# Kernel tuning notes

Hardware: AMD Instinct MI355X
Metric: run time of the kernel (lower is better)

The kernel has to match this reference:

```python
import jax, jax.numpy as jnp
import numpy as np

N, E, F, D, H, HID, OUT, G = 25000, 400000, 128, 16, 64, 128, 32, 64

def silu(v):
    return v * jax.nn.sigmoid(v)

def setup_inputs() -> dict:
    key = jax.random.key(0)
    ks = jax.random.split(key, 32)
    inp = {
        'x': jax.random.normal(ks[0], (N, F), jnp.float32),
        'pos': jax.random.normal(ks[1], (N, 3), jnp.float32),
        'edge_attr': jax.random.normal(ks[2], (E, D), jnp.float32),
        'edge_index': jax.random.randint(ks[3], (2, E), 0, N, jnp.int64),
        'batch': jnp.sort(jax.random.randint(ks[4], (N,), 0, G, jnp.int64)),
    }
    def lin(k, fan_in, fan_out):
        return jax.random.normal(k, (fan_in, fan_out), jnp.float32) / np.sqrt(fan_in)
    i = 5
    for l, in_c in enumerate([F, HID]):
        cat = 2 * in_c + D + 1
        inp[f'l{l}_mlp_w'] = lin(ks[i], cat, H); i += 1
        inp[f'l{l}_edge_w'] = lin(ks[i], H, H); i += 1
        inp[f'l{l}_edge_b'] = jnp.zeros((H,), jnp.float32)
        inp[f'l{l}_coord_w'] = lin(ks[i], H, 1); i += 1
        inp[f'l{l}_coord_b'] = jnp.zeros((1,), jnp.float32)
        inp[f'l{l}_node_w1'] = lin(ks[i], in_c + H, H); i += 1
        inp[f'l{l}_node_b1'] = jnp.zeros((H,), jnp.float32)
        inp[f'l{l}_node_w2'] = lin(ks[i], H, HID); i += 1
        inp[f'l{l}_node_b2'] = jnp.zeros((HID,), jnp.float32)
    inp['out_w1'] = lin(ks[i], HID, HID); i += 1
    inp['out_b1'] = jnp.zeros((HID,), jnp.float32)
    inp['out_w2'] = lin(ks[i], HID, OUT); i += 1
    inp['out_b2'] = jnp.zeros((OUT,), jnp.float32)
    return inp

def egnn_layer(x, pos, src, dst, edge_attr, mlp_w, edge_w, edge_b, coord_w, coord_b, nw1, nb1, nw2, nb2):
    # PyG flow source_to_target: i = dst (edge_index[1]), j = src (edge_index[0])
    diff = pos[dst] - pos[src]                    # (E,3)
    radial = jnp.sum(diff * diff, axis=1, keepdims=True)  # (E,1)
    cat = jnp.concatenate([x[dst], x[src], edge_attr, radial], axis=1)
    h = silu(cat @ mlp_w)                         # (E,H)
    e_ij = silu(h @ edge_w + edge_b)              # (E,H)
    coord_update = diff * silu(e_ij @ coord_w + coord_b)  # (E,3)
    e_agg = jax.ops.segment_sum(e_ij, dst, num_segments=N)          # sum reduce
    cu_sum = jax.ops.segment_sum(coord_update, dst, num_segments=N)
    deg = jax.ops.segment_sum(jnp.ones((E, 1), x.dtype), dst, num_segments=N)
    cu_mean = cu_sum / jnp.maximum(deg, 1.0)      # mean reduce, 0 for isolated nodes
    h_node = silu(jnp.concatenate([x, e_agg], axis=1) @ nw1 + nb1) @ nw2 + nb2
    return h_node, pos + cu_mean

def reference(x, pos, edge_attr, edge_index, batch,
              l0_mlp_w, l0_edge_w, l0_edge_b, l0_coord_w, l0_coord_b, l0_node_w1, l0_node_b1, l0_node_w2, l0_node_b2,
              l1_mlp_w, l1_edge_w, l1_edge_b, l1_coord_w, l1_coord_b, l1_node_w1, l1_node_b1, l1_node_w2, l1_node_b2,
              out_w1, out_b1, out_w2, out_b2):
    src, dst = edge_index[0], edge_index[1]
    x, pos = egnn_layer(x, pos, src, dst, edge_attr, l0_mlp_w, l0_edge_w, l0_edge_b, l0_coord_w, l0_coord_b, l0_node_w1, l0_node_b1, l0_node_w2, l0_node_b2)
    x, pos = egnn_layer(x, pos, src, dst, edge_attr, l1_mlp_w, l1_edge_w, l1_edge_b, l1_coord_w, l1_coord_b, l1_node_w1, l1_node_b1, l1_node_w2, l1_node_b2)
    # graph mean pooling over batch assignment
    g_sum = jax.ops.segment_sum(x, batch, num_segments=G)
    g_cnt = jax.ops.segment_sum(jnp.ones((N, 1), x.dtype), batch, num_segments=G)
    g = g_sum / jnp.maximum(g_cnt, 1.0)           # (G, HID)
    g = jax.nn.relu(g)
    return jax.nn.relu(g @ out_w1 + out_b1) @ out_w2 + out_b2  # (G, OUT)
```

## Files before the change

kernel.cpp:

```cpp
#include <hip/hip_runtime.h>
#include <math.h>

#define NN 25000
#define EE 400000
#define FF 128
#define DD 16
#define HH 64
#define HIDC 128
#define OUTC 32
#define GG 64
#define NODEBLK 782
#define SCATBLK 1563
#define NTILES 1563

#define EDGEBLK 1792
#define EW_Q 3
#define EW_R 3496

#define WQ_NW1 0
#define WQ_NW2 24576
#define WQ_WN  40960
#define WQ_EW  73728
#define WQ_W3  77824
#define WQ_LAYER 81920

typedef __attribute__((ext_vector_type(8))) short short8;
typedef __attribute__((ext_vector_type(8))) unsigned short u16x8;
typedef __attribute__((ext_vector_type(4))) float f32x4;

union S8 { short8 v; unsigned short u[8]; };
union U8 { u16x8 v; unsigned short u[8]; };

__device__ __forceinline__ float silu_f(float v) {
    return v / (1.f + __expf(-v));
}

__device__ __forceinline__ unsigned short f2bf_rne(float f) {
  unsigned u = __float_as_uint(f);
  unsigned r = u + 0x7fffu + ((u >> 16) & 1u);
  return (unsigned short)(r >> 16);
}
__device__ __forceinline__ float bfbits2f(unsigned short b) {
  return __uint_as_float(((unsigned)b) << 16);
}

__device__ __forceinline__ void split8(const float* hv, S8& hi, S8& lo) {
#pragma unroll
  for (int j = 0; j < 8; ++j) {
    const unsigned short hb = (unsigned short)(__float_as_uint(hv[j]) >> 16);
    hi.u[j] = hb;
    lo.u[j] = f2bf_rne(hv[j] - bfbits2f(hb));
  }
}

__device__ __forceinline__ f32x4 mfma3(const S8& ah, const S8& al,
                                       const S8& bh, const S8& bl, f32x4 c) {
  c = __builtin_amdgcn_mfma_f32_16x16x32_bf16(ah.v, bh.v, c, 0, 0, 0);
  c = __builtin_amdgcn_mfma_f32_16x16x32_bf16(al.v, bh.v, c, 0, 0, 0);
  c = __builtin_amdgcn_mfma_f32_16x16x32_bf16(ah.v, bl.v, c, 0, 0, 0);
  return c;
}

__device__ __forceinline__ void prepSplit(unsigned short* dst, const float* __restrict__ W,
                                          int ldw, int k0, int n0, int q, int m, int lane) {
  S8 hi, lo;
#pragma unroll
  for (int j = 0; j < 8; ++j) {
    const float wv = W[(size_t)(k0 + q * 8 + j) * ldw + n0 + m];
    const unsigned short hb = (unsigned short)(__float_as_uint(wv) >> 16);
    hi.u[j] = hb;
    lo.u[j] = f2bf_rne(wv - bfbits2f(hb));
  }
  *(short8*)(dst + lane * 8) = hi.v;
  *(short8*)(dst + 512 + lane * 8) = lo.v;
}

__device__ __forceinline__ void prepB16(unsigned short* dst, const float* __restrict__ W,
                                        int ldw, int k0, int n0, int q, int m, int lane,
                                        bool zero) {
  S8 b;
#pragma unroll
  for (int j = 0; j < 8; ++j)
    b.u[j] = zero ? (unsigned short)0
                  : f2bf_rne(W[(size_t)(k0 + q * 8 + j) * ldw + n0 + m]);
  *(short8*)(dst + lane * 8) = b.v;
}

__global__ __launch_bounds__(256) void k_hist(
    const int* __restrict__ ei, int* __restrict__ cnt,
    const float* __restrict__ nw1_0, const float* __restrict__ nw2_0,
    const float* __restrict__ mlp0, const float* __restrict__ ew0,
    const float* __restrict__ nw1_1, const float* __restrict__ nw2_1,
    const float* __restrict__ mlp1, const float* __restrict__ ew1,
    unsigned short* __restrict__ wq) {
  if (blockIdx.x < SCATBLK) {
    const int t = blockIdx.x * 256 + threadIdx.x;
    if (t < EE) atomicAdd(&cnt[ei[EE + t]], 1);
    return;
  }
  const int l = blockIdx.x - SCATBLK;
  const float* nw1 = l ? nw1_1 : nw1_0;
  const float* nw2 = l ? nw2_1 : nw2_0;
  const float* mlw = l ? mlp1 : mlp0;
  const float* ew  = l ? ew1 : ew0;
  unsigned short* base = wq + (size_t)l * WQ_LAYER;
  const int tid = threadIdx.x, w = tid >> 6, lane = tid & 63;
  const int q = lane >> 4, m = lane & 15;
  for (int f = w; f < 24; f += 4)
    prepSplit(base + WQ_NW1 + f * 1024, nw1, 64, (f % 6) * 32, (f / 6) * 16, q, m, lane);
  for (int f = w; f < 16; f += 4)
    prepSplit(base + WQ_NW2 + f * 1024, nw2, 128, (f & 1) * 32, (f >> 1) * 16, q, m, lane);
  if (l == 0) {
    for (int f = w; f < 32; f += 4) {
      const int nc = f >> 2, kc = f & 3;
      prepSplit(base + WQ_WN + f * 1024, mlp1 + (size_t)(nc < 4 ? 0 : 128 * 64), 64,
                kc * 32, (nc & 3) * 16, q, m, lane);
    }
  }
  for (int f = w; f < 8; f += 4)
    prepB16(base + WQ_EW + f * 512, ew, 64, (f >> 2) * 32, (f & 3) * 16, q, m, lane, false);
  for (int f = w; f < 4; f += 4)
    prepB16(base + WQ_W3 + f * 512, mlw + 256 * 64, 64, 0, f * 16, q, m, lane, lane >= 32);
}

__global__ __launch_bounds__(1024) void k_scan(
    const int* __restrict__ cnt, int* __restrict__ row_ptr, int* __restrict__ next) {
  __shared__ int s[1024];
  const int t = threadIdx.x;
  const int base = t * 25;
  int loc[25];
  int sum = 0;
#pragma unroll
  for (int i = 0; i < 25; ++i) {
    const int n = base + i;
    loc[i] = (n < NN) ? cnt[n] : 0;
    sum += loc[i];
  }
  s[t] = sum;
  __syncthreads();
  for (int off = 1; off < 1024; off <<= 1) {
    const int v = (t >= off) ? s[t - off] : 0;
    __syncthreads();
    s[t] += v;
    __syncthreads();
  }
  int run = s[t] - sum;
#pragma unroll
  for (int i = 0; i < 25; ++i) {
    const int n = base + i;
    if (n < NN) {
      row_ptr[n] = run;
      next[n] = run;
      run += loc[i];
    }
  }
  if (t == 0) row_ptr[NN] = EE;
}

__global__ __launch_bounds__(256) void k_sp(
    const int* __restrict__ ei, int* __restrict__ next,
    int* __restrict__ sdst, int* __restrict__ ssrc, int* __restrict__ seid,
    const float* __restrict__ X, const float* __restrict__ W,
    float* __restrict__ P1, unsigned short* __restrict__ P2h) {
  __shared__ __align__(16) float xT[4][128 * 12];
  if (blockIdx.x >= NODEBLK) {
    const int t = (blockIdx.x - NODEBLK) * 256 + threadIdx.x;
    if (t < EE) {
      const int d = ei[EE + t];
      const int slot = atomicAdd(&next[d], 1);
      sdst[slot] = d;
      ssrc[slot] = ei[t];
      seid[slot] = t;
    }
    return;
  }
  const int w = threadIdx.x >> 6, lane = threadIdx.x & 63;
  float* xt = xT[w];
  const int nb = (blockIdx.x * 4 + w) * 8;
#pragma unroll
  for (int e = 0; e < 8; ++e) {
    const int n = nb + e;
    const bool v = n < NN;
    xt[lane * 12 + e]        = v ? X[n * FF + lane] : 0.f;
    xt[(lane + 64) * 12 + e] = v ? X[n * FF + 64 + lane] : 0.f;
  }
  __syncthreads();
  float a1[8], a2[8];
#pragma unroll
  for (int e = 0; e < 8; ++e) { a1[e] = 0.f; a2[e] = 0.f; }
#pragma unroll 4
  for (int k = 0; k < 128; ++k) {
    const float wa = W[k * 64 + lane];
    const float wb = W[(128 + k) * 64 + lane];
    float xk[8];
    *(f32x4*)&xk[0] = *(const f32x4*)&xt[k * 12];
    *(f32x4*)&xk[4] = *(const f32x4*)&xt[k * 12 + 4];
#pragma unroll
    for (int e = 0; e < 8; ++e) {
      a1[e] = fmaf(xk[e], wa, a1[e]);
      a2[e] = fmaf(xk[e], wb, a2[e]);
    }
  }
#pragma unroll
  for (int e = 0; e < 8; ++e) {
    const int n = nb + e;
    if (n < NN) {
      P1[n * 64 + lane]  = a1[e];
      P2h[n * 64 + lane] = f2bf_rne(a2[e]);
    }
  }
}

template <bool COORD, bool GATHER>
__global__ __launch_bounds__(256, 4) void k_edge(
    const float* __restrict__ P1, const unsigned short* __restrict__ P2h,
    const float* __restrict__ pos, const float* __restrict__ eattr,
    unsigned short* __restrict__ seattr_h, const int* __restrict__ seid,
    const int* __restrict__ sdst, const int* __restrict__ ssrc,
    const unsigned short* __restrict__ wq, const float* __restrict__ mlp_w,
    const float* __restrict__ edge_b,
    const float* __restrict__ coord_w, const float* __restrict__ coord_b,
    float* __restrict__ e_agg, float* __restrict__ cu) {
  __shared__ __align__(16) float s_hs[4][16 * 76];
  __shared__ float s_diff[4][48];
  __shared__ float s_rad[4][16];
  __shared__ float s_red[4][16];
  const int tid = threadIdx.x, w = tid >> 6, lane = tid & 63;
  const int q = lane >> 4, m = lane & 15;

  S8 wB[2][4];
#pragma unroll
  for (int kc = 0; kc < 2; ++kc)
#pragma unroll
    for (int nc = 0; nc < 4; ++nc)
      wB[kc][nc].v = *(const short8*)(wq + WQ_EW + (kc * 4 + nc) * 512 + lane * 8);
  S8 w3B[4];
#pragma unroll
  for (int nc = 0; nc < 4; ++nc)
    w3B[nc].v = *(const short8*)(wq + WQ_W3 + nc * 512 + lane * 8);
  float w4r[4], cwr[4], ebr[4];
#pragma unroll
  for (int nc = 0; nc < 4; ++nc) {
    w4r[nc] = mlp_w[272 * 64 + nc * 16 + m];
    ebr[nc] = edge_b[nc * 16 + m];
    cwr[nc] = COORD ? coord_w[nc * 16 + m] : 0.f;
  }
  const float cb = COORD ? coord_b[0] : 0.f;

  const int wave_id = blockIdx.x * 4 + w;
  const int g0 = wave_id * EW_Q + (wave_id < EW_R ? wave_id : EW_R);
  const int ng = EW_Q + (wave_id < EW_R ? 1 : 0);

  const int pe = (lane < 48) ? (lane / 3) : 0;
  const int pc = lane - (lane / 3) * 3;

  int cur_dst = -1;
  float accum = 0.f;

  for (int g = 0; g < ng; ++g) {
    const int eb = (g0 + g) * 16;
    const int dm = sdst[eb + m];
    const int sm = ssrc[eb + m];
    f32x4 p1a[2], p1b[2];
    U8 p2r[2];
#pragma unroll
    for (int kc = 0; kc < 2; ++kc) {
      const float* pp1 = P1 + (size_t)dm * 64 + kc * 32 + q * 8;
      p1a[kc] = *(const f32x4*)pp1;
      p1b[kc] = *(const f32x4*)(pp1 + 4);
      p2r[kc].v = *(const u16x8*)(P2h + (size_t)sm * 64 + kc * 32 + q * 8);
    }
    if (lane < 48) {
      const int de = __shfl(dm, pe, 64), se = __shfl(sm, pe, 64);
      s_diff[w][lane] = pos[de * 3 + pc] - pos[se * 3 + pc];
    }
    S8 eaA;
#pragma unroll
    for (int j = 0; j < 8; ++j) eaA.u[j] = 0;
    if (lane < 32) {
      if (GATHER) {
        const int eid = seid[eb + m];
        const float* ep = &eattr[(size_t)eid * DD + q * 8];
        const f32x4 ea0 = *(const f32x4*)ep;
        const f32x4 ea1 = *(const f32x4*)(ep + 4);
#pragma unroll
        for (int j = 0; j < 4; ++j) {
          eaA.u[j]     = f2bf_rne(ea0[j]);
          eaA.u[4 + j] = f2bf_rne(ea1[j]);
        }
        *(short8*)&seattr_h[(size_t)(eb + m) * DD + q * 8] = eaA.v;
      } else {
        eaA.v = *(const short8*)&seattr_h[(size_t)(eb + m) * DD + q * 8];
      }
    }
    if (lane < 16) {
      const float d0 = s_diff[w][lane * 3 + 0];
      const float d1 = s_diff[w][lane * 3 + 1];
      const float d2 = s_diff[w][lane * 3 + 2];
      s_rad[w][lane] = fmaf(d0, d0, fmaf(d1, d1, d2 * d2));
    }
    float radr[4];
#pragma unroll
    for (int r = 0; r < 4; ++r) radr[r] = s_rad[w][q * 4 + r];
    f32x4 c3[4];
#pragma unroll
    for (int nc = 0; nc < 4; ++nc) {
      f32x4 z = {0.f, 0.f, 0.f, 0.f};
      c3[nc] = __builtin_amdgcn_mfma_f32_16x16x32_bf16(eaA.v, w3B[nc].v, z, 0, 0, 0);
    }
#pragma unroll
    for (int nc = 0; nc < 4; ++nc)
#pragma unroll
      for (int r = 0; r < 4; ++r)
        s_hs[w][(q * 4 + r) * 76 + nc * 16 + m] = fmaf(radr[r], w4r[nc], c3[nc][r]);
    S8 ahi[2], alo[2];
#pragma unroll
    for (int kc = 0; kc < 2; ++kc) {
      const float* hp = &s_hs[w][m * 76 + kc * 32 + q * 8];
      f32x4 h0 = *(const f32x4*)hp;
      f32x4 h1 = *(const f32x4*)(hp + 4);
      h0 = h0 + p1a[kc];
      h1 = h1 + p1b[kc];
      float hv[8];
      *(f32x4*)&hv[0] = h0;
      *(f32x4*)&hv[4] = h1;
#pragma unroll
      for (int j = 0; j < 8; ++j) {
        const float h = silu_f(hv[j] + bfbits2f(p2r[kc].u[j]));
        const unsigned short hb = (unsigned short)(__float_as_uint(h) >> 16);
        ahi[kc].u[j] = hb;
        alo[kc].u[j] = f2bf_rne(h - bfbits2f(hb));
      }
    }
    f32x4 o[4];
#pragma unroll
    for (int nc = 0; nc < 4; ++nc) {
      f32x4 bi = {ebr[nc], ebr[nc], ebr[nc], ebr[nc]};
      o[nc] = bi;
    }
#pragma unroll
    for (int kc = 0; kc < 2; ++kc)
#pragma unroll
      for (int nc = 0; nc < 4; ++nc) {
        o[nc] = __builtin_amdgcn_mfma_f32_16x16x32_bf16(ahi[kc].v, wB[kc][nc].v, o[nc], 0, 0, 0);
        o[nc] = __builtin_amdgcn_mfma_f32_16x16x32_bf16(alo[kc].v, wB[kc][nc].v, o[nc], 0, 0, 0);
      }
#pragma unroll
    for (int nc = 0; nc < 4; ++nc)
#pragma unroll
      for (int r = 0; r < 4; ++r) o[nc][r] = silu_f(o[nc][r]);
    if (COORD) {
#pragma unroll
      for (int r = 0; r < 4; ++r) {
        float v = o[0][r] * cwr[0] + o[1][r] * cwr[1] + o[2][r] * cwr[2] + o[3][r] * cwr[3];
        v += __shfl_xor(v, 1, 64);
        v += __shfl_xor(v, 2, 64);
        v += __shfl_xor(v, 4, 64);
        v += __shfl_xor(v, 8, 64);
        if (m == 0) s_red[w][q * 4 + r] = v;
      }
    }
#pragma unroll
    for (int nc = 0; nc < 4; ++nc)
#pragma unroll
      for (int r = 0; r < 4; ++r)
        s_hs[w][(q * 4 + r) * 76 + nc * 16 + m] = o[nc][r];
    for (int e = 0; e < 16; ++e) {
      const int dv = __shfl(dm, e, 64);
      const float v = s_hs[w][e * 76 + lane];
      if (dv == cur_dst) {
        accum += v;
      } else {
        if (cur_dst >= 0) atomicAdd(&e_agg[(size_t)cur_dst * 64 + lane], accum);
        cur_dst = dv;
        accum = v;
      }
    }
    if (COORD) {
      if (lane < 48) {
        const float s = silu_f(s_red[w][pe] + cb);
        atomicAdd(&cu[(size_t)__shfl(dm, pe, 64) * 3 + pc], s_diff[w][lane] * s);
      }
    }
  }
  if (cur_dst >= 0) atomicAdd(&e_agg[(size_t)cur_dst * 64 + lane], accum);
}

template <bool L0>
__global__ __launch_bounds__(256) void k_node(
    const float* __restrict__ x_in, float* __restrict__ e_agg,
    const unsigned short* __restrict__ wq,
    const float* __restrict__ nb1, const float* __restrict__ nb2,
    const float* __restrict__ pos_in, const float* __restrict__ cu,
    const int* __restrict__ row_ptr,
    float* __restrict__ x_out, float* __restrict__ pos_out,
    float* __restrict__ P1, unsigned short* __restrict__ P2h,
    const int* __restrict__ batch,
    float* __restrict__ g_sum, float* __restrict__ g_cnt) {
  __shared__ __align__(16) float sbuf[4][16 * 132];
  const int tid = threadIdx.x, w = tid >> 6, lane = tid & 63;
  const int q = lane >> 4, m = lane & 15;
  const int tile = blockIdx.x * 4 + w;
  if (tile >= NTILES) return;
  const int n0 = tile * 16;
  const int nm = n0 + m;
  const bool vm = nm < NN;
  float* sb = sbuf[w];

  S8 axh[6], axl[6];
#pragma unroll
  for (int kc = 0; kc < 6; ++kc) {
    float hv[8] = {0.f, 0.f, 0.f, 0.f, 0.f, 0.f, 0.f, 0.f};
    if (vm) {
      const float* src = (kc < 4) ? (x_in + (size_t)nm * HIDC + kc * 32 + q * 8)
                                  : (e_agg + (size_t)nm * 64 + (kc - 4) * 32 + q * 8);
      *(f32x4*)&hv[0] = *(const f32x4*)src;
      *(f32x4*)&hv[4] = *(const f32x4*)(src + 4);
    }
    split8(hv, axh[kc], axl[kc]);
  }
  if (L0 && vm) {
    const f32x4 z = {0.f, 0.f, 0.f, 0.f};
    float* ez = e_agg + (size_t)nm * 64 + q * 8;
    *(f32x4*)ez = z; *(f32x4*)(ez + 4) = z;
    *(f32x4*)(ez + 32) = z; *(f32x4*)(ez + 36) = z;
  }
#pragma unroll
  for (int nc = 0; nc < 4; ++nc) {
    const float b = nb1[nc * 16 + m];
    f32x4 acc = {b, b, b, b};
#pragma unroll
    for (int kc = 0; kc < 6; ++kc) {
      S8 bh, bl;
      const unsigned short* fb = wq + WQ_NW1 + (nc * 6 + kc) * 1024 + lane * 8;
      bh.v = *(const short8*)fb;
      bl.v = *(const short8*)(fb + 512);
      acc = mfma3(axh[kc], axl[kc], bh, bl, acc);
    }
#pragma unroll
    for (int r = 0; r < 4; ++r)
      sb[(q * 4 + r) * 132 + nc * 16 + m] = silu_f(acc[r]);
  }
  S8 ah[2], al[2];
#pragma unroll
  for (int kc = 0; kc < 2; ++kc) {
    float hv[8];
    const float* hp = &sb[m * 132 + kc * 32 + q * 8];
    *(f32x4*)&hv[0] = *(const f32x4*)hp;
    *(f32x4*)&hv[4] = *(const f32x4*)(hp + 4);
    split8(hv, ah[kc], al[kc]);
  }
  f32x4 hh[8];
#pragma unroll
  for (int nc = 0; nc < 8; ++nc) {
    const float b = nb2[nc * 16 + m];
    f32x4 acc = {b, b, b, b};
#pragma unroll
    for (int kc = 0; kc < 2; ++kc) {
      S8 bh, bl;
      const unsigned short* fb = wq + WQ_NW2 + (nc * 2 + kc) * 1024 + lane * 8;
      bh.v = *(const short8*)fb;
      bl.v = *(const short8*)(fb + 512);
      acc = mfma3(ah[kc], al[kc], bh, bl, acc);
    }
    hh[nc] = acc;
  }
  if (L0) {
#pragma unroll
    for (int nc = 0; nc < 8; ++nc)
#pragma unroll
      for (int r = 0; r < 4; ++r) {
        const int n = n0 + q * 4 + r;
        sb[(q * 4 + r) * 132 + nc * 16 + m] = hh[nc][r];
        if (n < NN) x_out[(size_t)n * HIDC + nc * 16 + m] = hh[nc][r];
      }
    if (lane < 48) {
      const int pe2 = lane / 3, pc2 = lane - pe2 * 3;
      const int n = n0 + pe2;
      if (n < NN) {
        const float dg = fmaxf((float)(row_ptr[n + 1] - row_ptr[n]), 1.f);
        pos_out[n * 3 + pc2] = pos_in[n * 3 + pc2] + cu[n * 3 + pc2] / dg;
      }
    }
    S8 a1h[4], a1l[4];
#pragma unroll
    for (int kc = 0; kc < 4; ++kc) {
      float hv[8];
      const float* hp = &sb[m * 132 + kc * 32 + q * 8];
      *(f32x4*)&hv[0] = *(const f32x4*)hp;
      *(f32x4*)&hv[4] = *(const f32x4*)(hp + 4);
      split8(hv, a1h[kc], a1l[kc]);
    }
#pragma unroll
    for (int nc = 0; nc < 8; ++nc) {
      const int ncc = nc & 3;
      f32x4 acc = {0.f, 0.f, 0.f, 0.f};
#pragma unroll
      for (int kc = 0; kc < 4; ++kc) {
        S8 bh, bl;
        const unsigned short* fb = wq + WQ_WN + (nc * 4 + kc) * 1024 + lane * 8;
        bh.v = *(const short8*)fb;
        bl.v = *(const short8*)(fb + 512);
        acc = mfma3(a1h[kc], a1l[kc], bh, bl, acc);
      }
#pragma unroll
      for (int r = 0; r < 4; ++r) {
        const int n = n0 + q * 4 + r;
        if (n < NN) {
          if (nc < 4) P1[(size_t)n * 64 + ncc * 16 + m] = acc[r];
          else        P2h[(size_t)n * 64 + ncc * 16 + m] = f2bf_rne(acc[r]);
        }
      }
    }
  } else {
    int curb = -1;
    float cnt2 = 0.f;
    float pacc[8];
#pragma unroll
    for (int r = 0; r < 4; ++r) {
      const int n = n0 + q * 4 + r;
      if (n < NN) {
        const int bg = batch[n];
        if (bg != curb) {
          if (curb >= 0) {
#pragma unroll
            for (int nc = 0; nc < 8; ++nc)
              atomicAdd(&g_sum[curb * HIDC + nc * 16 + m], pacc[nc]);
            if (m == 0) atomicAdd(&g_cnt[curb], cnt2);
          }
          curb = bg;
#pragma unroll
          for (int nc = 0; nc < 8; ++nc) pacc[nc] = hh[nc][r];
          cnt2 = 1.f;
        } else {
#pragma unroll
          for (int nc = 0; nc < 8; ++nc) pacc[nc] += hh[nc][r];
          cnt2 += 1.f;
        }
      }
    }
    if (curb >= 0) {
#pragma unroll
      for (int nc = 0; nc < 8; ++nc)
        atomicAdd(&g_sum[curb * HIDC + nc * 16 + m], pacc[nc]);
      if (m == 0) atomicAdd(&g_cnt[curb], cnt2);
    }
  }
}

__global__ __launch_bounds__(128) void k_final(
    const float* __restrict__ g_sum, const float* __restrict__ g_cnt,
    const float* __restrict__ w1, const float* __restrict__ b1,
    const float* __restrict__ w2, const float* __restrict__ b2,
    float* __restrict__ out) {
  __shared__ float sg[128];
  __shared__ float sh[128];
  const int g = blockIdx.x, j = threadIdx.x;
  const float c = fmaxf(g_cnt[g], 1.f);
  sg[j] = fmaxf(g_sum[g * HIDC + j] / c, 0.f);
  __syncthreads();
  float a = b1[j];
  for (int k = 0; k < 128; ++k) a += sg[k] * w1[k * 128 + j];
  sh[j] = fmaxf(a, 0.f);
  __syncthreads();
  if (j < OUTC) {
    float o = b2[j];
    for (int k = 0; k < 128; ++k) o += sh[k] * w2[k * OUTC + j];
    out[g * OUTC + j] = o;
  }
}

extern "C" void kernel_launch(void* const* d_in, const int* in_sizes, int n_in,
                              void* d_out, int out_size, void* d_ws, size_t ws_size,
                              hipStream_t stream) {
  const float* x     = (const float*)d_in[0];
  const float* pos   = (const float*)d_in[1];
  const float* eattr = (const float*)d_in[2];
  const int*   ei    = (const int*)d_in[3];
  const int*   batch = (const int*)d_in[4];
  const float* mlp_w[2]   = {(const float*)d_in[5],  (const float*)d_in[14]};
  const float* edge_w[2]  = {(const float*)d_in[6],  (const float*)d_in[15]};
  const float* edge_b[2]  = {(const float*)d_in[7],  (const float*)d_in[16]};
  const float* coord_w[2] = {(const float*)d_in[8],  (const float*)d_in[17]};
  const float* coord_b[2] = {(const float*)d_in[9],  (const float*)d_in[18]};
  const float* nw1[2]     = {(const float*)d_in[10], (const float*)d_in[19]};
  const float* nb1[2]     = {(const float*)d_in[11], (const float*)d_in[20]};
  const float* nw2[2]     = {(const float*)d_in[12], (const float*)d_in[21]};
  const float* nb2[2]     = {(const float*)d_in[13], (const float*)d_in[22]};
  const float* ow1 = (const float*)d_in[23];
  const float* ob1 = (const float*)d_in[24];
  const float* ow2 = (const float*)d_in[25];
  const float* ob2 = (const float*)d_in[26];
  float* out = (float*)d_out;

  char* p = (char*)d_ws;
  auto alloc = [&](size_t bytes) {
    void* r = (void*)p;
    p += (bytes + 255) & ~(size_t)255;
    return r;
  };
  float* P1            = (float*)alloc((size_t)NN * 64 * 4);
  unsigned short* P2h  = (unsigned short*)alloc((size_t)NN * 64 * 2);
  char* zero_base      = p;
  float* e_agg         = (float*)alloc((size_t)NN * 64 * 4);
  float* cu            = (float*)alloc((size_t)NN * 3 * 4);
  float* g_sum         = (float*)alloc((size_t)GG * HIDC * 4);
  float* g_cnt         = (float*)alloc((size_t)GG * 4);
  int* cnt             = (int*)alloc((size_t)NN * 4);
  const size_t zero_sz = (size_t)(p - zero_base);
  int* row_ptr         = (int*)alloc((size_t)(NN + 1) * 4);
  int* nxt             = (int*)alloc((size_t)NN * 4);
  int* sdst            = (int*)alloc((size_t)EE * 4);
  int* ssrc            = (int*)alloc((size_t)EE * 4);
  int* seid            = (int*)alloc((size_t)EE * 4);
  unsigned short* seah = (unsigned short*)alloc((size_t)EE * DD * 2);
  float* x1            = (float*)alloc((size_t)NN * HIDC * 4);
  float* pos1          = (float*)alloc((size_t)NN * 3 * 4);
  unsigned short* wqb  = (unsigned short*)alloc((size_t)2 * WQ_LAYER * 2);

  const int nodeTileBlk = (NTILES + 3) / 4;

  (void)hipMemsetAsync(zero_base, 0, zero_sz, stream);

  k_hist<<<SCATBLK + 2, 256, 0, stream>>>(ei, cnt,
      nw1[0], nw2[0], mlp_w[0], edge_w[0],
      nw1[1], nw2[1], mlp_w[1], edge_w[1], wqb);
  k_scan<<<1, 1024, 0, stream>>>(cnt, row_ptr, nxt);
  k_sp<<<NODEBLK + SCATBLK, 256, 0, stream>>>(ei, nxt, sdst, ssrc, seid,
      x, mlp_w[0], P1, P2h);

  k_edge<true, true><<<EDGEBLK, 256, 0, stream>>>(P1, P2h, pos, eattr,
      seah, seid, sdst, ssrc, wqb, mlp_w[0], edge_b[0],
      coord_w[0], coord_b[0], e_agg, cu);
  k_node<true><<<nodeTileBlk, 256, 0, stream>>>(x, e_agg, wqb, nb1[0], nb2[0],
      pos, cu, row_ptr, x1, pos1, P1, P2h, batch, g_sum, g_cnt);

  k_edge<false, false><<<EDGEBLK, 256, 0, stream>>>(P1, P2h, pos1, eattr,
      seah, seid, sdst, ssrc, wqb + WQ_LAYER, mlp_w[1], edge_b[1],
      coord_w[1], coord_b[1], e_agg, cu);
  k_node<false><<<nodeTileBlk, 256, 0, stream>>>(x1, e_agg, wqb + WQ_LAYER,
      nb1[1], nb2[1], pos1, cu, row_ptr, x1, pos1, P1, P2h,
      batch, g_sum, g_cnt);

  k_final<<<GG, 128, 0, stream>>>(g_sum, g_cnt, ow1, ob1, ow2, ob2, out);
}
```

Baseline: 456.4 us.

## Split node MLP columns across waves, retune edge kernel grid and LDS stride

The node kernel now gives each 16-node tile to a whole block: each of the four waves computes one 16-column slice of the first layer and two slices of the second, sharing the hidden activations through LDS with barriers. This launches four times as many node blocks with less per-wave serial MFMA work. The edge kernel gets more blocks (2048), launch bounds targeting 8 blocks per SM, a blockIdx swizzle across 8 groups (likely XCD-aware), and a tighter LDS row stride of 68. The costs are extra barriers, more redundant A-operand loads per block, and possible register spills from the tighter launch bounds.

After: 664.3 us. 1.46x slower.

```diff
diff --git a/kernel.cpp b/kernel.cpp
--- a/kernel.cpp
+++ b/kernel.cpp
@@ -13,9 +13,10 @@
 #define SCATBLK 1563
 #define NTILES 1563
 
-#define EDGEBLK 1792
+#define EDGEBLK 2048
 #define EW_Q 3
-#define EW_R 3496
+#define EW_R 424
+#define HS_STRIDE 68
 
 #define WQ_NW1 0
 #define WQ_NW2 24576
@@ -212,7 +213,7 @@
 }
 
 template <bool COORD, bool GATHER>
-__global__ __launch_bounds__(256, 4) void k_edge(
+__global__ __launch_bounds__(256, 8) void k_edge(
     const float* __restrict__ P1, const unsigned short* __restrict__ P2h,
     const float* __restrict__ pos, const float* __restrict__ eattr,
     unsigned short* __restrict__ seattr_h, const int* __restrict__ seid,
@@ -221,7 +222,7 @@
     const float* __restrict__ edge_b,
     const float* __restrict__ coord_w, const float* __restrict__ coord_b,
     float* __restrict__ e_agg, float* __restrict__ cu) {
-  __shared__ __align__(16) float s_hs[4][16 * 76];
+  __shared__ __align__(16) float s_hs[4][16 * HS_STRIDE];
   __shared__ float s_diff[4][48];
   __shared__ float s_rad[4][16];
   __shared__ float s_red[4][16];
@@ -247,7 +248,8 @@
   }
   const float cb = COORD ? coord_b[0] : 0.f;
 
-  const int wave_id = blockIdx.x * 4 + w;
+  const int sbid = (blockIdx.x & 7) * (EDGEBLK / 8) + (blockIdx.x >> 3);
+  const int wave_id = sbid * 4 + w;
   const int g0 = wave_id * EW_Q + (wave_id < EW_R ? wave_id : EW_R);
   const int ng = EW_Q + (wave_id < EW_R ? 1 : 0);
 
@@ -312,11 +314,11 @@
     for (int nc = 0; nc < 4; ++nc)
 #pragma unroll
       for (int r = 0; r < 4; ++r)
-        s_hs[w][(q * 4 + r) * 76 + nc * 16 + m] = fmaf(radr[r], w4r[nc], c3[nc][r]);
+        s_hs[w][(q * 4 + r) * HS_STRIDE + nc * 16 + m] = fmaf(radr[r], w4r[nc], c3[nc][r]);
     S8 ahi[2], alo[2];
 #pragma unroll
     for (int kc = 0; kc < 2; ++kc) {
-      const float* hp = &s_hs[w][m * 76 + kc * 32 + q * 8];
+      const float* hp = &s_hs[w][m * HS_STRIDE + kc * 32 + q * 8];
       f32x4 h0 = *(const f32x4*)hp;
       f32x4 h1 = *(const f32x4*)(hp + 4);
       h0 = h0 + p1a[kc];
@@ -364,10 +366,10 @@
     for (int nc = 0; nc < 4; ++nc)
 #pragma unroll
       for (int r = 0; r < 4; ++r)
-        s_hs[w][(q * 4 + r) * 76 + nc * 16 + m] = o[nc][r];
+        s_hs[w][(q * 4 + r) * HS_STRIDE + nc * 16 + m] = o[nc][r];
     for (int e = 0; e < 16; ++e) {
       const int dv = __shfl(dm, e, 64);
-      const float v = s_hs[w][e * 76 + lane];
+      const float v = s_hs[w][e * HS_STRIDE + lane];
       if (dv == cur_dst) {
         accum += v;
       } else {
@@ -397,15 +399,12 @@
     float* __restrict__ P1, unsigned short* __restrict__ P2h,
     const int* __restrict__ batch,
     float* __restrict__ g_sum, float* __restrict__ g_cnt) {
-  __shared__ __align__(16) float sbuf[4][16 * 132];
+  __shared__ __align__(16) float sb[16 * 132];
   const int tid = threadIdx.x, w = tid >> 6, lane = tid & 63;
   const int q = lane >> 4, m = lane & 15;
-  const int tile = blockIdx.x * 4 + w;
-  if (tile >= NTILES) return;
-  const int n0 = tile * 16;
+  const int n0 = blockIdx.x * 16;
   const int nm = n0 + m;
   const bool vm = nm < NN;
-  float* sb = sbuf[w];
 
   S8 axh[6], axl[6];
 #pragma unroll
@@ -419,27 +418,27 @@
     }
     split8(hv, axh[kc], axl[kc]);
   }
-  if (L0 && vm) {
+  {
+    const float b = nb1[w * 16 + m];
+    f32x4 acc = {b, b, b, b};
+#pragma unroll
+    for (int kc = 0; kc < 6; ++kc) {
+      S8 bh, bl;
+      const unsigned short* fb = wq + WQ_NW1 + (w * 6 + kc) * 1024 + lane * 8;
+      bh.v = *(const short8*)fb;
+      bl.v = *(const short8*)(fb + 512);
+      acc = mfma3(axh[kc], axl[kc], bh, bl, acc);
+    }
+#pragma unroll
+    for (int r = 0; r < 4; ++r)
+      sb[(q * 4 + r) * 132 + w * 16 + m] = silu_f(acc[r]);
+  }
+  __syncthreads();
+  if (L0 && vm && w == 3) {
     const f32x4 z = {0.f, 0.f, 0.f, 0.f};
     float* ez = e_agg + (size_t)nm * 64 + q * 8;
     *(f32x4*)ez = z; *(f32x4*)(ez + 4) = z;
     *(f32x4*)(ez + 32) = z; *(f32x4*)(ez + 36) = z;
-  }
-#pragma unroll
-  for (int nc = 0; nc < 4; ++nc) {
-    const float b = nb1[nc * 16 + m];
-    f32x4 acc = {b, b, b, b};
-#pragma unroll
-    for (int kc = 0; kc < 6; ++kc) {
-      S8 bh, bl;
-      const unsigned short* fb = wq + WQ_NW1 + (nc * 6 + kc) * 1024 + lane * 8;
-      bh.v = *(const short8*)fb;
-      bl.v = *(const short8*)(fb + 512);
-      acc = mfma3(axh[kc], axl[kc], bh, bl, acc);
-    }
-#pragma unroll
-    for (int r = 0; r < 4; ++r)
-      sb[(q * 4 + r) * 132 + nc * 16 + m] = silu_f(acc[r]);
   }
   S8 ah[2], al[2];
 #pragma unroll
@@ -450,9 +449,10 @@
     *(f32x4*)&hv[4] = *(const f32x4*)(hp + 4);
     split8(hv, ah[kc], al[kc]);
   }
-  f32x4 hh[8];
-#pragma unroll
-  for (int nc = 0; nc < 8; ++nc) {
+  f32x4 hh[2];
+#pragma unroll
+  for (int i = 0; i < 2; ++i) {
+    const int nc = w + i * 4;
     const float b = nb2[nc * 16 + m];
     f32x4 acc = {b, b, b, b};
 #pragma unroll
@@ -463,18 +463,21 @@
       bl.v = *(const short8*)(fb + 512);
       acc = mfma3(ah[kc], al[kc], bh, bl, acc);
     }
-    hh[nc] = acc;
+    hh[i] = acc;
   }
   if (L0) {
-#pragma unroll
-    for (int nc = 0; nc < 8; ++nc)
+    __syncthreads();
+#pragma unroll
+    for (int i = 0; i < 2; ++i) {
+      const int nc = w + i * 4;
 #pragma unroll
       for (int r = 0; r < 4; ++r) {
         const int n = n0 + q * 4 + r;
-        sb[(q * 4 + r) * 132 + nc * 16 + m] = hh[nc][r];
-        if (n < NN) x_out[(size_t)n * HIDC + nc * 16 + m] = hh[nc][r];
-      }
-    if (lane < 48) {
+        sb[(q * 4 + r) * 132 + nc * 16 + m] = hh[i][r];
+        if (n < NN) x_out[(size_t)n * HIDC + nc * 16 + m] = hh[i][r];
+      }
+    }
+    if (w == 0 && lane < 48) {
       const int pe2 = lane / 3, pc2 = lane - pe2 * 3;
       const int n = n0 + pe2;
       if (n < NN) {
@@ -482,6 +485,7 @@
         pos_out[n * 3 + pc2] = pos_in[n * 3 + pc2] + cu[n * 3 + pc2] / dg;
       }
     }
+    __syncthreads();
     S8 a1h[4], a1l[4];
 #pragma unroll
     for (int kc = 0; kc < 4; ++kc) {
@@ -492,8 +496,8 @@
       split8(hv, a1h[kc], a1l[kc]);
     }
 #pragma unroll
-    for (int nc = 0; nc < 8; ++nc) {
-      const int ncc = nc & 3;
+    for (int i = 0; i < 2; ++i) {
+      const int nc = w + i * 4;
       f32x4 acc = {0.f, 0.f, 0.f, 0.f};
 #pragma unroll
       for (int kc = 0; kc < 4; ++kc) {
@@ -507,15 +511,15 @@
       for (int r = 0; r < 4; ++r) {
         const int n = n0 + q * 4 + r;
         if (n < NN) {
-          if (nc < 4) P1[(size_t)n * 64 + ncc * 16 + m] = acc[r];
-          else        P2h[(size_t)n * 64 + ncc * 16 + m] = f2bf_rne(acc[r]);
+          if (i == 0) P1[(size_t)n * 64 + w * 16 + m] = acc[r];
+          else        P2h[(size_t)n * 64 + w * 16 + m] = f2bf_rne(acc[r]);
         }
       }
     }
   } else {
     int curb = -1;
     float cnt2 = 0.f;
-    float pacc[8];
+    float pacc[2];
 #pragma unroll
     for (int r = 0; r < 4; ++r) {
       const int n = n0 + q * 4 + r;
@@ -524,26 +528,26 @@
         if (bg != curb) {
           if (curb >= 0) {
 #pragma unroll
-            for (int nc = 0; nc < 8; ++nc)
-              atomicAdd(&g_sum[curb * HIDC + nc * 16 + m], pacc[nc]);
-            if (m == 0) atomicAdd(&g_cnt[curb], cnt2);
+            for (int i = 0; i < 2; ++i)
+              atomicAdd(&g_sum[curb * HIDC + (w + i * 4) * 16 + m], pacc[i]);
+            if (w == 0 && m == 0) atomicAdd(&g_cnt[curb], cnt2);
           }
           curb = bg;
-#pragma unroll
-          for (int nc = 0; nc < 8; ++nc) pacc[nc] = hh[nc][r];
+          pacc[0] = hh[0][r];
+          pacc[1] = hh[1][r];
           cnt2 = 1.f;
         } else {
-#pragma unroll
-          for (int nc = 0; nc < 8; ++nc) pacc[nc] += hh[nc][r];
+          pacc[0] += hh[0][r];
+          pacc[1] += hh[1][r];
           cnt2 += 1.f;
         }
       }
     }
     if (curb >= 0) {
 #pragma unroll
-      for (int nc = 0; nc < 8; ++nc)
-        atomicAdd(&g_sum[curb * HIDC + nc * 16 + m], pacc[nc]);
-      if (m == 0) atomicAdd(&g_cnt[curb], cnt2);
+      for (int i = 0; i < 2; ++i)
+        atomicAdd(&g_sum[curb * HIDC + (w + i * 4) * 16 + m], pacc[i]);
+      if (w == 0 && m == 0) atomicAdd(&g_cnt[curb], cnt2);
     }
   }
 }
@@ -618,8 +622,6 @@
   float* pos1          = (float*)alloc((size_t)NN * 3 * 4);
   unsigned short* wqb  = (unsigned short*)alloc((size_t)2 * WQ_LAYER * 2);
 
-  const int nodeTileBlk = (NTILES + 3) / 4;
-
   (void)hipMemsetAsync(zero_base, 0, zero_sz, stream);
 
   k_hist<<<SCATBLK + 2, 256, 0, stream>>>(ei, cnt,
@@ -632,13 +634,13 @@
   k_edge<true, true><<<EDGEBLK, 256, 0, stream>>>(P1, P2h, pos, eattr,
       seah, seid, sdst, ssrc, wqb, mlp_w[0], edge_b[0],
       coord_w[0], coord_b[0], e_agg, cu);
-  k_node<true><<<nodeTileBlk, 256, 0, stream>>>(x, e_agg, wqb, nb1[0], nb2[0],
+  k_node<true><<<NTILES, 256, 0, stream>>>(x, e_agg, wqb, nb1[0], nb2[0],
       pos, cu, row_ptr, x1, pos1, P1, P2h, batch, g_sum, g_cnt);
 
   k_edge<false, false><<<EDGEBLK, 256, 0, stream>>>(P1, P2h, pos1, eattr,
       seah, seid, sdst, ssrc, wqb + WQ_LAYER, mlp_w[1], edge_b[1],
       coord_w[1], coord_b[1], e_agg, cu);
-  k_node<false><<<nodeTileBlk, 256, 0, stream>>>(x1, e_agg, wqb + WQ_LAYER,
+  k_node<false><<<NTILES, 256, 0, stream>>>(x1, e_agg, wqb + WQ_LAYER,
       nb1[1], nb2[1], pos1, cu, row_ptr, x1, pos1, P1, P2h,
       batch, g_sum, g_cnt);
 
```
